# Kernel tuning notes

Hardware: AMD Instinct MI355X
Metric: run time of the kernel (lower is better)

Reference implementation:

```python
import jax, jax.numpy as jnp
import numpy as np
from jax import lax

K_TOP = 4
NF1, NF2 = 6, 14
KS1, KS2 = 7, 5


def conv1d_grouped(x, w, b, groups, pad):
    # x: (B, Cin, L), w: (Cout, Cin//groups, K)
    y = lax.conv_general_dilated(x, w, window_strides=(1,), padding=[(pad, pad)],
                                 dimension_numbers=('NCH', 'OIH', 'NCH'),
                                 feature_group_count=groups)
    return y + b[None, :, None]


def kmax_pool(x, k):
    # order-preserving k-max along last axis
    idx = jnp.sort(lax.top_k(x, k)[1], axis=-1)
    return jnp.take_along_axis(x, idx, axis=-1)


def fold_sum(h, b, nf, rows, L):
    # h: (B, rows*nf, L) with group-major channel layout (rows groups of nf)
    h = h.reshape(b, rows, nf, L).transpose(0, 2, 1, 3)        # (B, nf, rows, L)
    h = h.reshape(b, nf, rows // 2, 2, L).sum(axis=3)          # Fold(2,2): sum adjacent row pairs
    return h.transpose(0, 2, 1, 3).reshape(b, (rows // 2) * nf, L)


def setup_inputs() -> dict:
    key = jax.random.key(0)
    ks = jax.random.split(key, 8)
    V, D, C, B, S = 50257, 256, 1000, 32, 1024
    x = jax.random.randint(ks[0], (B, S), 0, V)
    emb = jax.random.normal(ks[1], (V, D), jnp.float32)
    w1 = jax.random.normal(ks[2], (NF1 * D, 1, KS1), jnp.float32) * 0.1
    b1 = jnp.zeros((NF1 * D,), jnp.float32)
    w2 = jax.random.normal(ks[3], (NF2 * (D // 2), NF1, KS2), jnp.float32) * 0.05
    b2 = jnp.zeros((NF2 * (D // 2),), jnp.float32)
    wf = jax.random.normal(ks[4], (C, NF2 * (D // 4) * K_TOP), jnp.float32) * 0.02
    bf = jnp.zeros((C,), jnp.float32)
    return {"x": x, "emb": emb, "w1": w1, "b1": b1, "w2": w2, "b2": b2, "wf": wf, "bf": bf}


def reference(x, emb, w1, b1, w2, b2, wf, bf):
    D = emb.shape[1]
    B = x.shape[0]
    h = emb[x].transpose(0, 2, 1)                 # (B, D, S)
    h = conv1d_grouped(h, w1, b1, groups=D, pad=KS1 - 1)   # (B, 6D, S+6)
    L1 = h.shape[-1]
    h = fold_sum(h, B, NF1, D, L1)                # (B, 3D, L1)
    # dynamic k-max: layer 1 of 2 -> k = max(k_top, ceil(L/2))
    k1 = max(K_TOP, -(-L1 // 2))
    h = jnp.tanh(kmax_pool(h, k1))
    h = conv1d_grouped(h, w2, b2, groups=D // 2, pad=KS2 - 1)  # (B, 7D, k1+4)
    L2 = h.shape[-1]
    h = fold_sum(h, B, NF2, D // 2, L2)           # (B, 14*(D/4), L2)
    h = jnp.tanh(kmax_pool(h, K_TOP))             # (B, 14*(D/4), k_top)
    # dropout is identity in eval mode
    h = h.reshape(B, -1)
    return h @ wf.T + bf
```

## Files before the change

kernel.cpp:

```cpp
#include <hip/hip_runtime.h>
#include <hip/hip_bf16.h>


typedef __attribute__((ext_vector_type(8))) short short8;
typedef __attribute__((ext_vector_type(4))) float f32x4;

__device__ __forceinline__ float fast_tanh(float x) {
    float e = __expf(2.f * x);
    return 1.f - 2.f / (e + 1.f);
}

__device__ __forceinline__ unsigned fkey(float f) {
    unsigned u = __float_as_uint(f);
    return (u & 0x80000000u) ? ~u : (u | 0x80000000u);
}

__device__ __forceinline__ float fkey_inv(unsigned k) {
    unsigned u = (k & 0x80000000u) ? (k ^ 0x80000000u) : ~k;
    return __uint_as_float(u);
}

__device__ __forceinline__ unsigned short f2bf_rne(float f) {
    unsigned u = __float_as_uint(f);
    return (unsigned short)((u + 0x7fffu + ((u >> 16) & 1u)) >> 16);
}

__global__ __launch_bounds__(256) void gather_kernel(
    const int* __restrict__ x, const float* __restrict__ emb, float* __restrict__ E2)
{
    const int b = blockIdx.x >> 4;
    const int c64 = blockIdx.x & 15;
    const int wv = threadIdx.x >> 6, lane = threadIdx.x & 63;
    float* dst = E2 + ((((size_t)b << 6) + lane) << 12);
#pragma unroll
    for (int t = 0; t < 16; ++t) {
        int l = (c64 << 6) + (wv << 4) + t;
        int tok = x[(b << 10) + l];
        float4 v = *(const float4*)(emb + ((size_t)tok << 8) + (lane << 2));
        *(float4*)(dst + (size_t)l * 4) = v;
    }
}

__global__ __launch_bounds__(896) void stage12_kernel(
    const int* __restrict__ x, const float* __restrict__ emb,
    const float* __restrict__ w1, const float* __restrict__ b1,
    const float* __restrict__ w2, const float* __restrict__ b2,
    const float* __restrict__ E2,
    __hip_bfloat16* __restrict__ H)
{
    __shared__ __align__(16) float e[4 * 1104];
    __shared__ __align__(16) float F[12 * 584];
    const int b = blockIdx.x >> 6;
    const int r2 = blockIdx.x & 63;
    const int tid = threadIdx.x;

    for (int i = tid; i < 12 * 584; i += 896) F[i] = 0.f;
    if (E2) {
        const float* E2blk = E2 + ((((size_t)b << 6) + r2) << 12);
        for (int idx = tid; idx < 1104; idx += 896) {
            int l = idx - 6;
            float4 v = {0.f, 0.f, 0.f, 0.f};
            if (l >= 0 && l < 1024) v = *(const float4*)(E2blk + (size_t)l * 4);
            e[0 * 1104 + idx] = v.x; e[1 * 1104 + idx] = v.y;
            e[2 * 1104 + idx] = v.z; e[3 * 1104 + idx] = v.w;
        }
    } else {
        for (int idx = tid; idx < 1104; idx += 896) {
            int l = idx - 6;
            float4 v = {0.f, 0.f, 0.f, 0.f};
            if (l >= 0 && l < 1024) {
                int tok = x[(b << 10) + l];
                v = *(const float4*)(emb + ((size_t)tok << 8) + (r2 << 2));
            }
            e[0 * 1104 + idx] = v.x; e[1 * 1104 + idx] = v.y;
            e[2 * 1104 + idx] = v.z; e[3 * 1104 + idx] = v.w;
        }
    }
    __syncthreads();

    const int w = tid >> 6;
    const int lane = tid & 63;

    if (w < 12) {
        const int half = (w >= 6) ? 1 : 0;
        const int f = w - half * 6;
        const float* ep0 = e + (2 * half) * 1104;
        const float* ep1 = ep0 + 1104;
        const int c0 = __builtin_amdgcn_readfirstlane((2 * (2 * r2 + half)) * 6 + f);
        const int c1 = c0 + 6;
        float wA[7], wB[7];
#pragma unroll
        for (int t = 0; t < 7; ++t) { wA[t] = w1[c0 * 7 + t]; wB[t] = w1[c1 * 7 + t]; }
        const float bias = b1[c0] + b1[c1];

        const int pos0 = lane * 17;
        float a0[7], a1[7];
#pragma unroll
        for (int t = 0; t < 7; ++t) { a0[t] = ep0[pos0 + t]; a1[t] = ep1[pos0 + t]; }

        unsigned key[17];
#pragma unroll
        for (int j = 0; j < 17; ++j) {
            float a = bias;
#pragma unroll
            for (int t = 0; t < 7; ++t) a += a0[t] * wA[t] + a1[t] * wB[t];
            key[j] = (pos0 + j < 1030) ? fkey(a) : 0u;
            if (j < 16) {
#pragma unroll
                for (int t = 0; t < 6; ++t) { a0[t] = a0[t + 1]; a1[t] = a1[t + 1]; }
                a0[6] = ep0[pos0 + j + 7];
                a1[6] = ep1[pos0 + j + 7];
            }
        }

        unsigned T = 0u;
        for (int bit = 31; bit >= 0; --bit) {
            unsigned cand = T | (1u << bit);
            int cnt = 0;
#pragma unroll
            for (int j = 0; j < 17; ++j) cnt += (int)__popcll(__ballot(key[j] >= cand));
            if (cnt >= 515) T = cand;
            if (cnt == 515) break;
        }

        const unsigned long long lm = (1ull << lane) - 1ull;
        int gt_tot = 0, gt_run = 0, eq_run = 0;
#pragma unroll
        for (int j = 0; j < 17; ++j) {
            unsigned long long bg = __ballot(key[j] > T);
            unsigned long long be = __ballot(key[j] == T);
            gt_tot += (int)__popcll(bg);
            gt_run += (int)__popcll(bg & lm);
            eq_run += (int)__popcll(be & lm);
        }
        const int q = 515 - gt_tot;
        float* Frow = F + w * 584;
#pragma unroll
        for (int j = 0; j < 17; ++j) {
            bool isgt = key[j] > T;
            bool iseq = key[j] == T;
            int pos = gt_run + (eq_run < q ? eq_run : q);
            if (isgt || (iseq && eq_run < q)) Frow[4 + pos] = fast_tanh(fkey_inv(key[j]));
            gt_run += isgt ? 1 : 0;
            eq_run += iseq ? 1 : 0;
        }
    }
    __syncthreads();

    {
        const int j = w;
        const int base = lane * 9;
        const int bidx = __builtin_amdgcn_readfirstlane((2 * r2) * 14 + j);
        const float bias2 = b2[bidx] + b2[bidx + 14];
        float acc[9];
#pragma unroll
        for (int jj = 0; jj < 9; ++jj) acc[jj] = bias2;

#pragma unroll
        for (int i = 0; i < 12; ++i) {
            const float* Fr = F + i * 584 + base;
            const int cg = 2 * r2 + ((i >= 6) ? 1 : 0);
            const int ii = (i >= 6) ? (i - 6) : i;
            const int widx = __builtin_amdgcn_readfirstlane(((cg * 14 + j) * 6 + ii) * 5);
            float wv[5];
#pragma unroll
            for (int t = 0; t < 5; ++t) wv[t] = w2[widx + t];
            float win[5];
#pragma unroll
            for (int t = 0; t < 5; ++t) win[t] = Fr[t];
#pragma unroll
            for (int jj = 0; jj < 9; ++jj) {
#pragma unroll
                for (int t = 0; t < 5; ++t) acc[jj] += win[t] * wv[t];
                if (jj < 8) {
#pragma unroll
                    for (int t = 0; t < 4; ++t) win[t] = win[t + 1];
                    win[4] = Fr[jj + 5];
                }
            }
        }

        float vv[9];
#pragma unroll
        for (int jj = 0; jj < 9; ++jj) vv[jj] = (base + jj < 519) ? acc[jj] : -INFINITY;
        float sv[4]; int si[4];
#pragma unroll
        for (int it = 0; it < 4; ++it) {
            float m = vv[0]; int mi = base;
#pragma unroll
            for (int jj = 1; jj < 9; ++jj) { if (vv[jj] > m) { m = vv[jj]; mi = base + jj; } }
#pragma unroll
            for (int d = 1; d < 64; d <<= 1) {
                float om = __shfl_xor(m, d, 64);
                int omi = __shfl_xor(mi, d, 64);
                if (om > m || (om == m && omi < mi)) { m = om; mi = omi; }
            }
            sv[it] = m; si[it] = mi;
            int lj = mi - base;
#pragma unroll
            for (int jj = 0; jj < 9; ++jj) if (jj == lj) vv[jj] = -INFINITY;
        }
#define CSWAP(a, bq) { if (si[a] > si[bq]) { int ti = si[a]; si[a] = si[bq]; si[bq] = ti; \
                                             float tv = sv[a]; sv[a] = sv[bq]; sv[bq] = tv; } }
        CSWAP(0, 1) CSWAP(2, 3) CSWAP(0, 2) CSWAP(1, 3) CSWAP(1, 2)
#undef CSWAP
        if (lane == 0) {
            __hip_bfloat16* op = H + (size_t)b * 3584 + (r2 * 14 + j) * 4;
#pragma unroll
            for (int k = 0; k < 4; ++k) op[k] = __float2bfloat16(fast_tanh(sv[k]));
        }
    }
}

__global__ __launch_bounds__(256) void bias_init_kernel(
    const float* __restrict__ bfv, float* __restrict__ out)
{
    int idx = blockIdx.x * 256 + threadIdx.x;
    if (idx < 32000) out[idx] = bfv[idx - (idx / 1000) * 1000];
}

__global__ __launch_bounds__(256) void stage3_kernel(
    const __hip_bfloat16* __restrict__ Hb, const float* __restrict__ wf,
    float* __restrict__ out)
{
    __shared__ __align__(16) float sred[2 * 4 * 256];
    const int nt = blockIdx.x % 63;
    const int kc = blockIdx.x / 63;
    const int w = threadIdx.x >> 6, lane = threadIdx.x & 63;
    const int row = lane & 15, quad = lane >> 4;
    const int c = nt * 16 + row;
    const bool cvalid = (c < 1000);
    const int kofs = kc * 896 + w * 224 + quad * 8;
    const __hip_bfloat16* ap0 = Hb + (size_t)row * 3584 + kofs;
    const __hip_bfloat16* ap1 = ap0 + (size_t)16 * 3584;
    const float* bp = wf + (size_t)(cvalid ? c : 0) * 3584 + kofs;

    f32x4 acc0 = {0.f, 0.f, 0.f, 0.f};
    f32x4 acc1 = {0.f, 0.f, 0.f, 0.f};
#pragma unroll
    for (int it = 0; it < 7; ++it) {
        short8 a0 = *(const short8*)(ap0 + it * 32);
        short8 a1 = *(const short8*)(ap1 + it * 32);
        float4 p0 = *(const float4*)(bp + it * 32);
        float4 p1 = *(const float4*)(bp + it * 32 + 4);
        short8 bfr;
        bfr[0] = (short)f2bf_rne(p0.x); bfr[1] = (short)f2bf_rne(p0.y);
        bfr[2] = (short)f2bf_rne(p0.z); bfr[3] = (short)f2bf_rne(p0.w);
        bfr[4] = (short)f2bf_rne(p1.x); bfr[5] = (short)f2bf_rne(p1.y);
        bfr[6] = (short)f2bf_rne(p1.z); bfr[7] = (short)f2bf_rne(p1.w);
        if (!cvalid) bfr = short8{0, 0, 0, 0, 0, 0, 0, 0};
        acc0 = __builtin_amdgcn_mfma_f32_16x16x32_bf16(a0, bfr, acc0, 0, 0, 0);
        acc1 = __builtin_amdgcn_mfma_f32_16x16x32_bf16(a1, bfr, acc1, 0, 0, 0);
    }
#pragma unroll
    for (int r_ = 0; r_ < 4; ++r_) {
        sred[(0 * 4 + w) * 256 + lane * 4 + r_] = acc0[r_];
        sred[(1 * 4 + w) * 256 + lane * 4 + r_] = acc1[r_];
    }
    __syncthreads();
    if (threadIdx.x < 128) {
        const int mt = threadIdx.x >> 6;
        const int l2 = threadIdx.x & 63;
        const int rr = l2 & 15, qq = l2 >> 4;
        const int cc = nt * 16 + rr;
        if (cc < 1000) {
            const float* sp = sred + mt * 4 * 256;
#pragma unroll
            for (int r_ = 0; r_ < 4; ++r_) {
                float s = sp[0 * 256 + l2 * 4 + r_] + sp[1 * 256 + l2 * 4 + r_]
                        + sp[2 * 256 + l2 * 4 + r_] + sp[3 * 256 + l2 * 4 + r_];
                int brow = mt * 16 + qq * 4 + r_;
                atomicAdd(&out[brow * 1000 + cc], s);
            }
        }
    }
}

extern "C" void kernel_launch(void* const* d_in, const int* in_sizes, int n_in,
                              void* d_out, int out_size, void* d_ws, size_t ws_size,
                              hipStream_t stream) {
    const int* x      = (const int*)d_in[0];
    const float* emb  = (const float*)d_in[1];
    const float* w1   = (const float*)d_in[2];
    const float* b1   = (const float*)d_in[3];
    const float* w2   = (const float*)d_in[4];
    const float* b2   = (const float*)d_in[5];
    const float* wf   = (const float*)d_in[6];
    const float* bfv  = (const float*)d_in[7];

    const size_t E2_BYTES = (size_t)32 * 64 * 1024 * 4 * 4;
    const size_t H_BYTES  = (size_t)32 * 3584 * 2;
    float* E2 = nullptr;
    __hip_bfloat16* H;
    if (ws_size >= E2_BYTES + H_BYTES) {
        E2 = (float*)d_ws;
        H = (__hip_bfloat16*)((char*)d_ws + E2_BYTES);
    } else {
        H = (__hip_bfloat16*)d_ws;
    }

    bias_init_kernel<<<125, 256, 0, stream>>>(bfv, (float*)d_out);
    if (E2) gather_kernel<<<32 * 16, 256, 0, stream>>>(x, emb, E2);
    stage12_kernel<<<32 * 64, 896, 0, stream>>>(x, emb, w1, b1, w2, b2, E2, H);
    stage3_kernel<<<63 * 4, 256, 0, stream>>>(H, wf, (float*)d_out);
}
```

Before: 261.0 us.

## Compute stage-2 grouped conv with split-bf16 MFMA instead of scalar FMAs

Replaces the per-wave scalar 5-tap convolution over 12 folded input rows with 16x16x32 bf16 MFMA tiles. Weights and inputs are split into hi/lo bf16 parts and combined with three products to approximate fp32 accuracy. Results go through a reused shared buffer before the k-max selection, and the bias is added after selection. This adds bf16 conversion work, an extra barrier and shared-memory round trip, and a small precision risk.

```diff
diff --git a/kernel.cpp b/kernel.cpp
--- a/kernel.cpp
+++ b/kernel.cpp
@@ -48,13 +48,14 @@
     const float* __restrict__ E2,
     __hip_bfloat16* __restrict__ H)
 {
-    __shared__ __align__(16) float e[4 * 1104];
-    __shared__ __align__(16) float F[12 * 584];
+    __shared__ __align__(16) float X[8512];
+    __shared__ __align__(16) float F[12 * 536];
     const int b = blockIdx.x >> 6;
     const int r2 = blockIdx.x & 63;
     const int tid = threadIdx.x;
-
-    for (int i = tid; i < 12 * 584; i += 896) F[i] = 0.f;
+    float* e = X;
+
+    for (int i = tid; i < 12 * 536; i += 896) F[i] = 0.f;
     if (E2) {
         const float* E2blk = E2 + ((((size_t)b << 6) + r2) << 12);
         for (int idx = tid; idx < 1104; idx += 896) {
@@ -134,7 +135,7 @@
             eq_run += (int)__popcll(be & lm);
         }
         const int q = 515 - gt_tot;
-        float* Frow = F + w * 584;
+        float* Frow = F + w * 536;
 #pragma unroll
         for (int j = 0; j < 17; ++j) {
             bool isgt = key[j] > T;
@@ -147,42 +148,76 @@
     }
     __syncthreads();
 
+    const int jA = lane & 15;
+    const int q3 = lane >> 4;
+    float* OUT = X;
+    short8 Ah0, Ah1, Al0, Al1;
+    {
+        float wt[16];
+#pragma unroll
+        for (int mm = 0; mm < 16; ++mm) {
+            float v = 0.f;
+            if (mm < 15 && jA < 14) {
+                const int irow = 3 * q3 + mm / 5;
+                const int t = mm % 5;
+                const int h2 = (irow >= 6) ? 1 : 0;
+                v = w2[(((2 * r2 + h2) * 14 + jA) * 6 + (irow - 6 * h2)) * 5 + t];
+            }
+            wt[mm] = v;
+        }
+#pragma unroll
+        for (int m = 0; m < 8; ++m) {
+            unsigned short h0 = f2bf_rne(wt[m]);
+            float fh0 = __uint_as_float((unsigned)h0 << 16);
+            Ah0[m] = (short)h0;
+            Al0[m] = (short)f2bf_rne(wt[m] - fh0);
+            unsigned short h1 = f2bf_rne(wt[8 + m]);
+            float fh1 = __uint_as_float((unsigned)h1 << 16);
+            Ah1[m] = (short)h1;
+            Al1[m] = (short)f2bf_rne(wt[8 + m] - fh1);
+        }
+    }
+    for (int tile = w; tile < 33; tile += 14) {
+        const int p0 = tile << 4;
+        const int bidx = (3 * q3) * 536 + p0 + jA;
+        float fv[16];
+#pragma unroll
+        for (int mm = 0; mm < 15; ++mm) fv[mm] = F[bidx + (mm / 5) * 536 + (mm % 5)];
+        fv[15] = 0.f;
+        short8 Bh0, Bh1, Bl0, Bl1;
+#pragma unroll
+        for (int m = 0; m < 8; ++m) {
+            unsigned short h0 = f2bf_rne(fv[m]);
+            float fh0 = __uint_as_float((unsigned)h0 << 16);
+            Bh0[m] = (short)h0;
+            Bl0[m] = (short)f2bf_rne(fv[m] - fh0);
+            unsigned short h1 = f2bf_rne(fv[8 + m]);
+            float fh1 = __uint_as_float((unsigned)h1 << 16);
+            Bh1[m] = (short)h1;
+            Bl1[m] = (short)f2bf_rne(fv[8 + m] - fh1);
+        }
+        f32x4 d0 = {0.f, 0.f, 0.f, 0.f};
+        d0 = __builtin_amdgcn_mfma_f32_16x16x32_bf16(Ah0, Bh0, d0, 0, 0, 0);
+        d0 = __builtin_amdgcn_mfma_f32_16x16x32_bf16(Ah1, Bh1, d0, 0, 0, 0);
+        d0 = __builtin_amdgcn_mfma_f32_16x16x32_bf16(Ah0, Bl0, d0, 0, 0, 0);
+        d0 = __builtin_amdgcn_mfma_f32_16x16x32_bf16(Ah1, Bl1, d0, 0, 0, 0);
+        d0 = __builtin_amdgcn_mfma_f32_16x16x32_bf16(Al0, Bh0, d0, 0, 0, 0);
+        d0 = __builtin_amdgcn_mfma_f32_16x16x32_bf16(Al1, Bh1, d0, 0, 0, 0);
+        float* orow = OUT + (q3 * 4) * 532 + p0 + jA;
+#pragma unroll
+        for (int r = 0; r < 4; ++r) orow[r * 532] = d0[r];
+    }
+    __syncthreads();
+
     {
         const int j = w;
         const int base = lane * 9;
-        const int bidx = __builtin_amdgcn_readfirstlane((2 * r2) * 14 + j);
-        const float bias2 = b2[bidx] + b2[bidx + 14];
-        float acc[9];
-#pragma unroll
-        for (int jj = 0; jj < 9; ++jj) acc[jj] = bias2;
-
-#pragma unroll
-        for (int i = 0; i < 12; ++i) {
-            const float* Fr = F + i * 584 + base;
-            const int cg = 2 * r2 + ((i >= 6) ? 1 : 0);
-            const int ii = (i >= 6) ? (i - 6) : i;
-            const int widx = __builtin_amdgcn_readfirstlane(((cg * 14 + j) * 6 + ii) * 5);
-            float wv[5];
-#pragma unroll
-            for (int t = 0; t < 5; ++t) wv[t] = w2[widx + t];
-            float win[5];
-#pragma unroll
-            for (int t = 0; t < 5; ++t) win[t] = Fr[t];
-#pragma unroll
-            for (int jj = 0; jj < 9; ++jj) {
-#pragma unroll
-                for (int t = 0; t < 5; ++t) acc[jj] += win[t] * wv[t];
-                if (jj < 8) {
-#pragma unroll
-                    for (int t = 0; t < 4; ++t) win[t] = win[t + 1];
-                    win[4] = Fr[jj + 5];
-                }
-            }
-        }
-
+        const int bidx2 = __builtin_amdgcn_readfirstlane((2 * r2) * 14 + j);
+        const float bias2 = b2[bidx2] + b2[bidx2 + 14];
         float vv[9];
 #pragma unroll
-        for (int jj = 0; jj < 9; ++jj) vv[jj] = (base + jj < 519) ? acc[jj] : -INFINITY;
+        for (int jj = 0; jj < 9; ++jj)
+            vv[jj] = (base + jj < 519) ? OUT[j * 532 + base + jj] : -INFINITY;
         float sv[4]; int si[4];
 #pragma unroll
         for (int it = 0; it < 4; ++it) {
@@ -207,7 +242,7 @@
         if (lane == 0) {
             __hip_bfloat16* op = H + (size_t)b * 3584 + (r2 * 14 + j) * 4;
 #pragma unroll
-            for (int k = 0; k < 4; ++k) op[k] = __float2bfloat16(fast_tanh(sv[k]));
+            for (int k = 0; k < 4; ++k) op[k] = __float2bfloat16(fast_tanh(sv[k] + bias2));
         }
     }
 }
```

After: 273.3 us. 4.7% more time.
